# Kernel tuning notes

Measured on AMD Instinct MI355X. Metric: run time of the kernel, lower is better.

Reference implementation:

```python
import jax, jax.numpy as jnp
import numpy as np

# config constants (from pose_config)
GROUPS = [[0, 1, 2, 3, 4], [5, 6, 7, 8, 9, 10], [11, 12, 13, 14, 15, 16]]
NORM_SCALE = 1.0
OUT_H, OUT_W = 16, 8


def setup_inputs() -> dict:
    key = jax.random.key(0)
    x = jax.random.normal(key, (2048, 17, 64, 32), dtype=jnp.float32)
    return {"x": x}


def reference(x):
    n, c, _, _ = x.shape
    # bilinear, align_corners=False (half-pixel centers) == jax.image.resize 'linear'
    x = jax.image.resize(x, (n, c, OUT_H, OUT_W), method='linear')
    h, w = OUT_H, OUT_W

    x_flat = x.reshape(n, c, h * w)
    idx = jnp.argmax(x_flat, axis=2)                      # [n, c]
    max_response = jnp.max(x_flat, axis=2)                # [n, c]
    max_index = jnp.stack(
        [(idx % w).astype(jnp.float32), (idx // w).astype(jnp.float32)],
        axis=-1)                                          # [n, c, 2]

    # group-wise reduce (group_mode='sum'): sum heatmaps, mean of max responses
    heatmap = jnp.concatenate(
        [jnp.sum(x[:, g], axis=1, keepdims=True) for g in GROUPS], axis=1)   # [n, G, h, w]
    max_response_2 = jnp.concatenate(
        [jnp.mean(max_response[:, g], axis=1, keepdims=True) for g in GROUPS],
        axis=1)                                           # [n, G]

    # normalize: softmax over spatial dim
    g = heatmap.shape[1]
    heatmap = jax.nn.softmax(
        NORM_SCALE * heatmap.reshape(n, g, h * w), axis=2).reshape(n, g, h, w)

    return heatmap, max_response_2, max_index
```

## Files before the change

kernel.cpp:

```cpp
#include <hip/hip_runtime.h>
#include <math.h>

#define N_CH 17
#define IN_H 64
#define IN_W 32
#define HW 128

#define SIN_CH 2176
#define TMP_STRIDE 37
#define TMP_CH (16 * TMP_STRIDE)
#define EDGE (32.f / 28.f)

#define BAR_LGKM() asm volatile("s_waitcnt lgkmcnt(0)\n\ts_barrier" ::: "memory")

#define W0 (1.f/32.f)
#define W1 (3.f/32.f)
#define W2 (5.f/32.f)
#define W3 (7.f/32.f)

#define TAP8(b, R) (W0*(b)[(R)*32]     + W1*(b)[((R)+1)*32] + W2*(b)[((R)+2)*32] \
                  + W3*(b)[((R)+3)*32] + W3*(b)[((R)+4)*32] + W2*(b)[((R)+5)*32] \
                  + W1*(b)[((R)+6)*32] + W0*(b)[((R)+7)*32])

__global__ __launch_bounds__(256)
void heatmap_kernel(const float* __restrict__ x,
                    float* __restrict__ out_heat,
                    float* __restrict__ out_mr,
                    float* __restrict__ out_mi) {
    const int n = blockIdx.x;
    const int t = threadIdx.x;
    const int w = t >> 6, l = t & 63;
    const int half = t >> 7;
    const int tl = t & 127;
    const int col = tl & 31, q = tl >> 5;
    const int p = tl;
    const int r2 = p >> 3, oc = p & 7;
    const int hpos = w & 1;

    __shared__ float s_in[2 * SIN_CH];
    __shared__ float s_tmp[2 * TMP_CH];
    __shared__ float s_cval[N_CH * 2];
    __shared__ int   s_cidx[N_CH * 2];

    float* sw = s_in + half * SIN_CH;
    float* st = s_tmp + half * TMP_CH;

    s_in[half * SIN_CH + (tl < 64 ? tl : 2048 + tl)] = 0.f;
    if (t < 128) {
        int ch = t >> 6, rr = (t >> 2) & 15, jj = t & 3;
        int cc = (jj < 2) ? jj : jj + 32;
        s_tmp[ch * TMP_CH + rr * TMP_STRIDE + cc] = 0.f;
    }

    const float* xn = x + (size_t)n * N_CH * IN_H * IN_W;
    float ga0 = 0.f, ga1 = 0.f, ga2 = 0.f;

    float4 A0, A1, A2, A3, B0, B1, B2, B3;
    {
        const float4* src = (const float4*)(xn + (size_t)half * (IN_H * IN_W));
        A0 = src[tl]; A1 = src[tl + 128]; A2 = src[tl + 256]; A3 = src[tl + 384];
    }

#pragma unroll
    for (int i = 0; i < 9; ++i) {
        const int c = 2 * i + half;
        const bool valid = (c < N_CH);

        if (i < 8) {
            int cn = 2 * (i + 1) + half;
            if (cn > 16) cn = 16;
            const float4* src = (const float4*)(xn + (size_t)cn * (IN_H * IN_W));
            if (i & 1) { A0 = src[tl]; A1 = src[tl+128]; A2 = src[tl+256]; A3 = src[tl+384]; }
            else       { B0 = src[tl]; B1 = src[tl+128]; B2 = src[tl+256]; B3 = src[tl+384]; }
        }

        {
            float4* dst = (float4*)(sw + 64);
            dst[tl]       = (i & 1) ? B0 : A0;
            dst[tl + 128] = (i & 1) ? B1 : A1;
            dst[tl + 256] = (i & 1) ? B2 : A2;
            dst[tl + 384] = (i & 1) ? B3 : A3;
        }

        BAR_LGKM();

        const float* b = sw + (16 * q) * 32 + col;
        float o0 = TAP8(b, 0);
        float o1 = TAP8(b, 4);
        float o2 = TAP8(b, 8);
        float o3 = TAP8(b, 12);
        if (q == 0) o0 *= EDGE;
        if (q == 3) o3 *= EDGE;

        BAR_LGKM();

        st[(4 * q + 0) * TMP_STRIDE + 2 + col] = o0;
        st[(4 * q + 1) * TMP_STRIDE + 2 + col] = o1;
        st[(4 * q + 2) * TMP_STRIDE + 2 + col] = o2;
        st[(4 * q + 3) * TMP_STRIDE + 2 + col] = o3;

        const float* b2 = st + r2 * TMP_STRIDE + 4 * oc;
        float o = W0*b2[0] + W1*b2[1] + W2*b2[2] + W3*b2[3]
                + W3*b2[4] + W2*b2[5] + W1*b2[6] + W0*b2[7];
        if (oc == 0 || oc == 7) o *= EDGE;

        if (valid) {
            if (c < 5)       ga0 += o;
            else if (c < 11) ga1 += o;
            else             ga2 += o;

            float bv = o; int bi = p;
#pragma unroll
            for (int off = 32; off >= 1; off >>= 1) {
                float ov = __shfl_down(bv, off);
                int   oi = __shfl_down(bi, off);
                if (ov > bv || (ov == bv && oi < bi)) { bv = ov; bi = oi; }
            }
            if (l == 0) { s_cval[2 * c + hpos] = bv; s_cidx[2 * c + hpos] = bi; }
        }
    }

    __syncthreads();
    float* s_part = s_in;
    s_part[(half * 3 + 0) * HW + p] = ga0;
    s_part[(half * 3 + 1) * HW + p] = ga1;
    s_part[(half * 3 + 2) * HW + p] = ga2;
    __syncthreads();

    if (w < 3) {
        const int g = w;
        float v0 = s_part[g * HW + l]      + s_part[(3 + g) * HW + l];
        float v1 = s_part[g * HW + 64 + l] + s_part[(3 + g) * HW + 64 + l];
        float m = fmaxf(v0, v1);
#pragma unroll
        for (int off = 1; off < 64; off <<= 1) m = fmaxf(m, __shfl_xor(m, off));
        float e0 = expf(v0 - m), e1 = expf(v1 - m);
        float s = e0 + e1;
#pragma unroll
        for (int off = 1; off < 64; off <<= 1) s += __shfl_xor(s, off);
        float inv = 1.f / s;
        float* dsto = out_heat + ((size_t)n * 3 + g) * HW;
        dsto[l]      = e0 * inv;
        dsto[l + 64] = e1 * inv;
    } else {
        if (l < N_CH) {
            int c = l;
            float v0 = s_cval[2 * c], v1 = s_cval[2 * c + 1];
            int i0 = s_cidx[2 * c], i1 = s_cidx[2 * c + 1];
            int bi = (v1 > v0) ? i1 : i0;
            float* mi = out_mi + ((size_t)n * N_CH + c) * 2;
            mi[0] = (float)(bi & 7);
            mi[1] = (float)(bi >> 3);
        }
        if (l < 3) {
            int lo = (l == 0) ? 0 : ((l == 1) ? 5 : 11);
            int hi = (l == 0) ? 5 : ((l == 1) ? 11 : 17);
            float acc = 0.f;
            for (int c2 = lo; c2 < hi; ++c2)
                acc += fmaxf(s_cval[2 * c2], s_cval[2 * c2 + 1]);
            out_mr[(size_t)n * 3 + l] = acc / (float)(hi - lo);
        }
    }
}

extern "C" void kernel_launch(void* const* d_in, const int* in_sizes, int n_in,
                              void* d_out, int out_size, void* d_ws, size_t ws_size,
                              hipStream_t stream) {
    const float* x = (const float*)d_in[0];
    float* out = (float*)d_out;
    const int N = in_sizes[0] / (N_CH * IN_H * IN_W);
    float* out_heat = out;
    float* out_mr   = out_heat + (size_t)N * 3 * HW;
    float* out_mi   = out_mr + (size_t)N * 3;
    heatmap_kernel<<<dim3(N), dim3(256), 0, stream>>>(x, out_heat, out_mr, out_mi);
}
```

Measured before the change: 379.3 us.

## Stream input channels directly to LDS with double-buffered global_load_lds

Replaces the register-staged float4 prefetch and LDS store with direct global-to-LDS loads (global_load_lds, 16 bytes) into a double-buffered shared input array. Each barrier waits with vmcnt(4), so the current channel's loads have landed while the next channel's loads stay in flight. This removes VGPR staging and the explicit ds_write traffic, at the cost of doubling the input LDS footprint, which may lower occupancy. It also issues one extra redundant load on the final iteration.

Result: no change. 379.9 us (+0.2%).

```diff
diff --git a/kernel.cpp b/kernel.cpp
--- a/kernel.cpp
+++ b/kernel.cpp
@@ -11,8 +11,6 @@
 #define TMP_CH (16 * TMP_STRIDE)
 #define EDGE (32.f / 28.f)
 
-#define BAR_LGKM() asm volatile("s_waitcnt lgkmcnt(0)\n\ts_barrier" ::: "memory")
-
 #define W0 (1.f/32.f)
 #define W1 (3.f/32.f)
 #define W2 (5.f/32.f)
@@ -21,6 +19,15 @@
 #define TAP8(b, R) (W0*(b)[(R)*32]     + W1*(b)[((R)+1)*32] + W2*(b)[((R)+2)*32] \
                   + W3*(b)[((R)+3)*32] + W3*(b)[((R)+4)*32] + W2*(b)[((R)+5)*32] \
                   + W1*(b)[((R)+6)*32] + W0*(b)[((R)+7)*32])
+
+#define BAR_LGKM() asm volatile("s_waitcnt lgkmcnt(0)\n\ts_barrier" ::: "memory")
+#define BAR_VM4()  asm volatile("s_waitcnt vmcnt(4)\n\ts_barrier" ::: "memory")
+
+__device__ __forceinline__ void gll16(const float* g, float* l) {
+    __builtin_amdgcn_global_load_lds(
+        (const __attribute__((address_space(1))) void*)g,
+        (__attribute__((address_space(3))) void*)l, 16, 0, 0);
+}
 
 __global__ __launch_bounds__(256)
 void heatmap_kernel(const float* __restrict__ x,
@@ -37,28 +44,35 @@
     const int r2 = p >> 3, oc = p & 7;
     const int hpos = w & 1;
 
-    __shared__ float s_in[2 * SIN_CH];
+    __shared__ float s_in[2][2 * SIN_CH];
     __shared__ float s_tmp[2 * TMP_CH];
     __shared__ float s_cval[N_CH * 2];
     __shared__ int   s_cidx[N_CH * 2];
 
-    float* sw = s_in + half * SIN_CH;
     float* st = s_tmp + half * TMP_CH;
 
-    s_in[half * SIN_CH + (tl < 64 ? tl : 2048 + tl)] = 0.f;
+    {
+        int pb = t >> 7, ph = (t >> 6) & 1;
+        float* r = &s_in[pb][ph * SIN_CH];
+        r[l] = 0.f;
+        r[2112 + l] = 0.f;
+    }
     if (t < 128) {
         int ch = t >> 6, rr = (t >> 2) & 15, jj = t & 3;
         int cc = (jj < 2) ? jj : jj + 32;
         s_tmp[ch * TMP_CH + rr * TMP_STRIDE + cc] = 0.f;
     }
+    asm volatile("s_waitcnt lgkmcnt(0)" ::: "memory");
 
     const float* xn = x + (size_t)n * N_CH * IN_H * IN_W;
     float ga0 = 0.f, ga1 = 0.f, ga2 = 0.f;
 
-    float4 A0, A1, A2, A3, B0, B1, B2, B3;
     {
-        const float4* src = (const float4*)(xn + (size_t)half * (IN_H * IN_W));
-        A0 = src[tl]; A1 = src[tl + 128]; A2 = src[tl + 256]; A3 = src[tl + 384];
+        const float* src = xn + (size_t)half * 2048;
+        float* dst = &s_in[0][half * SIN_CH + 64];
+#pragma unroll
+        for (int j = 0; j < 4; ++j)
+            gll16(src + 4 * (tl + 128 * j), dst + 4 * (tl + 128 * j));
     }
 
 #pragma unroll
@@ -66,24 +80,19 @@
         const int c = 2 * i + half;
         const bool valid = (c < N_CH);
 
-        if (i < 8) {
+        {
             int cn = 2 * (i + 1) + half;
             if (cn > 16) cn = 16;
-            const float4* src = (const float4*)(xn + (size_t)cn * (IN_H * IN_W));
-            if (i & 1) { A0 = src[tl]; A1 = src[tl+128]; A2 = src[tl+256]; A3 = src[tl+384]; }
-            else       { B0 = src[tl]; B1 = src[tl+128]; B2 = src[tl+256]; B3 = src[tl+384]; }
+            const float* src = xn + (size_t)cn * 2048;
+            float* dst = &s_in[(i + 1) & 1][half * SIN_CH + 64];
+#pragma unroll
+            for (int j = 0; j < 4; ++j)
+                gll16(src + 4 * (tl + 128 * j), dst + 4 * (tl + 128 * j));
         }
 
-        {
-            float4* dst = (float4*)(sw + 64);
-            dst[tl]       = (i & 1) ? B0 : A0;
-            dst[tl + 128] = (i & 1) ? B1 : A1;
-            dst[tl + 256] = (i & 1) ? B2 : A2;
-            dst[tl + 384] = (i & 1) ? B3 : A3;
-        }
+        BAR_VM4();
 
-        BAR_LGKM();
-
+        const float* sw = &s_in[i & 1][half * SIN_CH];
         const float* b = sw + (16 * q) * 32 + col;
         float o0 = TAP8(b, 0);
         float o1 = TAP8(b, 4);
@@ -121,7 +130,7 @@
     }
 
     __syncthreads();
-    float* s_part = s_in;
+    float* s_part = &s_in[0][0];
     s_part[(half * 3 + 0) * HW + p] = ga0;
     s_part[(half * 3 + 1) * HW + p] = ga1;
     s_part[(half * 3 + 2) * HW + p] = ga2;
```

## Process one channel per wavefront to drop block barriers in resize loop

Applied to the files above, without the earlier changes.

Restructures the work split so each of the four wavefronts handles a whole channel (channels w, w+4, ...) with its own private LDS buffers, instead of two 128-thread halves sharing a channel. This removes the two block-wide barriers per iteration, because all LDS exchange now stays inside a single wavefront. Each thread computes twice as many outputs and writes the argmax results directly. In exchange, LDS use doubles, the work is unbalanced across waves (17 channels over 4 waves gives one wave 5 channels and the rest 4), and register pressure rises from the 8 float4 prefetch registers. Correctness within a wave relies on implicit wavefront lockstep for LDS ordering.

Result: no change. 377.8 us (-0.4%).

```diff
diff --git a/kernel.cpp b/kernel.cpp
--- a/kernel.cpp
+++ b/kernel.cpp
@@ -2,16 +2,12 @@
 #include <math.h>
 
 #define N_CH 17
-#define IN_H 64
-#define IN_W 32
 #define HW 128
 
-#define SIN_CH 2176
+#define SIN_W 2176
 #define TMP_STRIDE 37
-#define TMP_CH (16 * TMP_STRIDE)
+#define TMP_W (16 * TMP_STRIDE)
 #define EDGE (32.f / 28.f)
-
-#define BAR_LGKM() asm volatile("s_waitcnt lgkmcnt(0)\n\ts_barrier" ::: "memory")
 
 #define W0 (1.f/32.f)
 #define W1 (3.f/32.f)
@@ -30,111 +26,124 @@
     const int n = blockIdx.x;
     const int t = threadIdx.x;
     const int w = t >> 6, l = t & 63;
-    const int half = t >> 7;
-    const int tl = t & 127;
-    const int col = tl & 31, q = tl >> 5;
-    const int p = tl;
-    const int r2 = p >> 3, oc = p & 7;
-    const int hpos = w & 1;
 
-    __shared__ float s_in[2 * SIN_CH];
-    __shared__ float s_tmp[2 * TMP_CH];
-    __shared__ float s_cval[N_CH * 2];
-    __shared__ int   s_cidx[N_CH * 2];
+    __shared__ float s_in[4 * SIN_W];
+    __shared__ float s_tmp[4 * TMP_W];
+    __shared__ float s_cval[N_CH];
 
-    float* sw = s_in + half * SIN_CH;
-    float* st = s_tmp + half * TMP_CH;
+    float* sw = s_in + w * SIN_W;
+    float* st = s_tmp + w * TMP_W;
 
-    s_in[half * SIN_CH + (tl < 64 ? tl : 2048 + tl)] = 0.f;
-    if (t < 128) {
-        int ch = t >> 6, rr = (t >> 2) & 15, jj = t & 3;
+    sw[l] = 0.f;
+    sw[2112 + l] = 0.f;
+    {
+        int rr = l >> 2, jj = l & 3;
         int cc = (jj < 2) ? jj : jj + 32;
-        s_tmp[ch * TMP_CH + rr * TMP_STRIDE + cc] = 0.f;
+        st[rr * TMP_STRIDE + cc] = 0.f;
     }
 
-    const float* xn = x + (size_t)n * N_CH * IN_H * IN_W;
-    float ga0 = 0.f, ga1 = 0.f, ga2 = 0.f;
+    const float* xn = x + (size_t)n * N_CH * 2048;
+    const int col = l & 31, h = l >> 5;
+    const int oc = l & 7;
+    const float cs2 = (oc == 0 || oc == 7) ? EDGE : 1.f;
 
-    float4 A0, A1, A2, A3, B0, B1, B2, B3;
+    float ga0l = 0.f, ga0h = 0.f, ga1l = 0.f, ga1h = 0.f, ga2l = 0.f, ga2h = 0.f;
+
+    float4 v0, v1, v2, v3, v4, v5, v6, v7;
     {
-        const float4* src = (const float4*)(xn + (size_t)half * (IN_H * IN_W));
-        A0 = src[tl]; A1 = src[tl + 128]; A2 = src[tl + 256]; A3 = src[tl + 384];
+        const float4* src = (const float4*)(xn + (size_t)w * 2048);
+        v0 = src[l];       v1 = src[l + 64];  v2 = src[l + 128]; v3 = src[l + 192];
+        v4 = src[l + 256]; v5 = src[l + 320]; v6 = src[l + 384]; v7 = src[l + 448];
     }
 
 #pragma unroll
-    for (int i = 0; i < 9; ++i) {
-        const int c = 2 * i + half;
-        const bool valid = (c < N_CH);
-
-        if (i < 8) {
-            int cn = 2 * (i + 1) + half;
-            if (cn > 16) cn = 16;
-            const float4* src = (const float4*)(xn + (size_t)cn * (IN_H * IN_W));
-            if (i & 1) { A0 = src[tl]; A1 = src[tl+128]; A2 = src[tl+256]; A3 = src[tl+384]; }
-            else       { B0 = src[tl]; B1 = src[tl+128]; B2 = src[tl+256]; B3 = src[tl+384]; }
-        }
+    for (int i = 0; i < 5; ++i) {
+        const int c = w + 4 * i;
+        if (c >= N_CH) break;
 
         {
             float4* dst = (float4*)(sw + 64);
-            dst[tl]       = (i & 1) ? B0 : A0;
-            dst[tl + 128] = (i & 1) ? B1 : A1;
-            dst[tl + 256] = (i & 1) ? B2 : A2;
-            dst[tl + 384] = (i & 1) ? B3 : A3;
+            dst[l]       = v0; dst[l + 64]  = v1; dst[l + 128] = v2; dst[l + 192] = v3;
+            dst[l + 256] = v4; dst[l + 320] = v5; dst[l + 384] = v6; dst[l + 448] = v7;
         }
 
-        BAR_LGKM();
+        if (c + 4 < N_CH) {
+            const float4* src = (const float4*)(xn + (size_t)(c + 4) * 2048);
+            v0 = src[l];       v1 = src[l + 64];  v2 = src[l + 128]; v3 = src[l + 192];
+            v4 = src[l + 256]; v5 = src[l + 320]; v6 = src[l + 384]; v7 = src[l + 448];
+        }
 
-        const float* b = sw + (16 * q) * 32 + col;
+        const float* b = sw + h * 1024 + col;
         float o0 = TAP8(b, 0);
         float o1 = TAP8(b, 4);
         float o2 = TAP8(b, 8);
         float o3 = TAP8(b, 12);
-        if (q == 0) o0 *= EDGE;
-        if (q == 3) o3 *= EDGE;
+        float o4 = TAP8(b, 16);
+        float o5 = TAP8(b, 20);
+        float o6 = TAP8(b, 24);
+        float o7 = TAP8(b, 28);
+        if (h == 0) o0 *= EDGE; else o7 *= EDGE;
 
-        BAR_LGKM();
+        float* tw = st + (8 * h) * TMP_STRIDE + 2 + col;
+        tw[0]               = o0;
+        tw[TMP_STRIDE]      = o1;
+        tw[2 * TMP_STRIDE]  = o2;
+        tw[3 * TMP_STRIDE]  = o3;
+        tw[4 * TMP_STRIDE]  = o4;
+        tw[5 * TMP_STRIDE]  = o5;
+        tw[6 * TMP_STRIDE]  = o6;
+        tw[7 * TMP_STRIDE]  = o7;
 
-        st[(4 * q + 0) * TMP_STRIDE + 2 + col] = o0;
-        st[(4 * q + 1) * TMP_STRIDE + 2 + col] = o1;
-        st[(4 * q + 2) * TMP_STRIDE + 2 + col] = o2;
-        st[(4 * q + 3) * TMP_STRIDE + 2 + col] = o3;
+        const float* b2 = st + (l >> 3) * TMP_STRIDE + 4 * oc;
+        float olo = W0*b2[0] + W1*b2[1] + W2*b2[2] + W3*b2[3]
+                  + W3*b2[4] + W2*b2[5] + W1*b2[6] + W0*b2[7];
+        const float* b3 = b2 + 8 * TMP_STRIDE;
+        float ohi = W0*b3[0] + W1*b3[1] + W2*b3[2] + W3*b3[3]
+                  + W3*b3[4] + W2*b3[5] + W1*b3[6] + W0*b3[7];
+        olo *= cs2; ohi *= cs2;
 
-        const float* b2 = st + r2 * TMP_STRIDE + 4 * oc;
-        float o = W0*b2[0] + W1*b2[1] + W2*b2[2] + W3*b2[3]
-                + W3*b2[4] + W2*b2[5] + W1*b2[6] + W0*b2[7];
-        if (oc == 0 || oc == 7) o *= EDGE;
+        if (c < 5)       { ga0l += olo; ga0h += ohi; }
+        else if (c < 11) { ga1l += olo; ga1h += ohi; }
+        else             { ga2l += olo; ga2h += ohi; }
 
-        if (valid) {
-            if (c < 5)       ga0 += o;
-            else if (c < 11) ga1 += o;
-            else             ga2 += o;
-
-            float bv = o; int bi = p;
+        {
+            float bv; int bi;
+            if (ohi > olo) { bv = ohi; bi = l + 64; } else { bv = olo; bi = l; }
 #pragma unroll
             for (int off = 32; off >= 1; off >>= 1) {
                 float ov = __shfl_down(bv, off);
                 int   oi = __shfl_down(bi, off);
                 if (ov > bv || (ov == bv && oi < bi)) { bv = ov; bi = oi; }
             }
-            if (l == 0) { s_cval[2 * c + hpos] = bv; s_cidx[2 * c + hpos] = bi; }
+            if (l == 0) {
+                s_cval[c] = bv;
+                float* mi = out_mi + ((size_t)n * N_CH + c) * 2;
+                mi[0] = (float)(bi & 7);
+                mi[1] = (float)(bi >> 3);
+            }
         }
     }
 
     __syncthreads();
     float* s_part = s_in;
-    s_part[(half * 3 + 0) * HW + p] = ga0;
-    s_part[(half * 3 + 1) * HW + p] = ga1;
-    s_part[(half * 3 + 2) * HW + p] = ga2;
+    s_part[(w * 3 + 0) * HW + l]      = ga0l;
+    s_part[(w * 3 + 0) * HW + l + 64] = ga0h;
+    s_part[(w * 3 + 1) * HW + l]      = ga1l;
+    s_part[(w * 3 + 1) * HW + l + 64] = ga1h;
+    s_part[(w * 3 + 2) * HW + l]      = ga2l;
+    s_part[(w * 3 + 2) * HW + l + 64] = ga2h;
     __syncthreads();
 
     if (w < 3) {
         const int g = w;
-        float v0 = s_part[g * HW + l]      + s_part[(3 + g) * HW + l];
-        float v1 = s_part[g * HW + 64 + l] + s_part[(3 + g) * HW + 64 + l];
-        float m = fmaxf(v0, v1);
+        float lo = s_part[(0 * 3 + g) * HW + l]      + s_part[(1 * 3 + g) * HW + l]
+                 + s_part[(2 * 3 + g) * HW + l]      + s_part[(3 * 3 + g) * HW + l];
+        float hi = s_part[(0 * 3 + g) * HW + l + 64] + s_part[(1 * 3 + g) * HW + l + 64]
+                 + s_part[(2 * 3 + g) * HW + l + 64] + s_part[(3 * 3 + g) * HW + l + 64];
+        float m = fmaxf(lo, hi);
 #pragma unroll
         for (int off = 1; off < 64; off <<= 1) m = fmaxf(m, __shfl_xor(m, off));
-        float e0 = expf(v0 - m), e1 = expf(v1 - m);
+        float e0 = expf(lo - m), e1 = expf(hi - m);
         float s = e0 + e1;
 #pragma unroll
         for (int off = 1; off < 64; off <<= 1) s += __shfl_xor(s, off);
@@ -142,24 +151,12 @@
         float* dsto = out_heat + ((size_t)n * 3 + g) * HW;
         dsto[l]      = e0 * inv;
         dsto[l + 64] = e1 * inv;
-    } else {
-        if (l < N_CH) {
-            int c = l;
-            float v0 = s_cval[2 * c], v1 = s_cval[2 * c + 1];
-            int i0 = s_cidx[2 * c], i1 = s_cidx[2 * c + 1];
-            int bi = (v1 > v0) ? i1 : i0;
-            float* mi = out_mi + ((size_t)n * N_CH + c) * 2;
-            mi[0] = (float)(bi & 7);
-            mi[1] = (float)(bi >> 3);
-        }
-        if (l < 3) {
-            int lo = (l == 0) ? 0 : ((l == 1) ? 5 : 11);
-            int hi = (l == 0) ? 5 : ((l == 1) ? 11 : 17);
-            float acc = 0.f;
-            for (int c2 = lo; c2 < hi; ++c2)
-                acc += fmaxf(s_cval[2 * c2], s_cval[2 * c2 + 1]);
-            out_mr[(size_t)n * 3 + l] = acc / (float)(hi - lo);
-        }
+    } else if (l < 3) {
+        int lo = (l == 0) ? 0 : ((l == 1) ? 5 : 11);
+        int hi = (l == 0) ? 5 : ((l == 1) ? 11 : 17);
+        float acc = 0.f;
+        for (int c2 = lo; c2 < hi; ++c2) acc += s_cval[c2];
+        out_mr[(size_t)n * 3 + l] = acc / (float)(hi - lo);
     }
 }
 
@@ -168,7 +165,7 @@
                               hipStream_t stream) {
     const float* x = (const float*)d_in[0];
     float* out = (float*)d_out;
-    const int N = in_sizes[0] / (N_CH * IN_H * IN_W);
+    const int N = in_sizes[0] / (N_CH * 64 * 32);
     float* out_heat = out;
     float* out_mr   = out_heat + (size_t)N * 3 * HW;
     float* out_mi   = out_mr + (size_t)N * 3;
```
